# Kernel tuning notes

Measured on AMD Instinct MI355X. Metric: run time of the kernel, lower is better.

The kernel has to match this reference:

```python
import jax, jax.numpy as jnp
import numpy as np

R_RAYS = 65536
S_PER_RAY = 128
N_TOTAL = R_RAYS * S_PER_RAY


def setup_inputs() -> dict:
    key = jax.random.key(0)
    k1, k2, k3, k4 = jax.random.split(key, 4)
    sigmas = jax.random.uniform(k1, (N_TOTAL,), dtype=jnp.float32) * 2.0  # densities >= 0
    rgbs = jax.random.uniform(k2, (N_TOTAL, 3), dtype=jnp.float32)
    deltas = jax.random.uniform(k3, (N_TOTAL,), dtype=jnp.float32) * 0.01 + 1e-3
    ts = jax.random.uniform(k4, (N_TOTAL,), dtype=jnp.float32) * 6.0 + 0.1
    ray_idx = jnp.arange(R_RAYS, dtype=jnp.int32)
    rays_a = jnp.stack([ray_idx, ray_idx * S_PER_RAY,
                        jnp.full((R_RAYS,), S_PER_RAY, dtype=jnp.int32)], axis=1)
    return {"sigmas": sigmas, "rgbs": rgbs, "deltas": deltas, "ts": ts,
            "rays_a": rays_a, "T_threshold": 1e-4}


def reference(sigmas, rgbs, deltas, ts, rays_a, T_threshold):
    R = rays_a.shape[0]
    N = sigmas.shape[0]
    S_max = int(jnp.max(rays_a[:, 2]))  # max samples per ray (concrete)

    offs = jnp.arange(S_max, dtype=rays_a.dtype)
    valid = offs[None, :] < rays_a[:, 2, None]              # [R, S] prefix mask
    idx = jnp.where(valid, rays_a[:, 1, None] + offs[None, :], N - 1)  # [R, S]

    a = 1.0 - jnp.exp(-sigmas[idx] * deltas[idx])           # [R, S] alphas

    # Sequential transmittance recurrence with early-exit (T set to 0 once below threshold)
    def step(T, xs):
        a_s, v_s = xs                                        # [R], [R]
        alive = (T > T_threshold) & v_s
        w = jnp.where(alive, a_s * T, 0.0)
        T = jnp.where(alive, T * (1.0 - a_s), 0.0)
        return T, (w, alive)

    T0 = jnp.ones((R,), sigmas.dtype)
    _, (wT, aliveT) = jax.lax.scan(step, T0, (a.T, valid.T))
    w = wT.T                                                 # [R, S] weights
    alive = aliveT.T

    op_n = jnp.sum(w, axis=1)                                # [R]
    dep_n = jnp.sum(w * ts[idx], axis=1)                     # [R]
    rgb_n = jnp.einsum('rs,rsc->rc', w, rgbs[idx])           # [R, 3]
    cnt_n = jnp.sum(alive, axis=1).astype(jnp.int32)

    ridx = rays_a[:, 0]
    opacity = jnp.zeros((R,), w.dtype).at[ridx].add(op_n)
    depth = jnp.zeros((R,), w.dtype).at[ridx].add(dep_n)
    rgb = jnp.zeros((R, 3), w.dtype).at[ridx].add(rgb_n)
    total_samples = jnp.zeros((R,), jnp.int32).at[ridx].add(cnt_n)
    # invalid slots were mapped to index N-1 with w=0, so .add is safe
    ws = jnp.zeros((N,), w.dtype).at[idx.reshape(-1)].add(w.reshape(-1))

    return total_samples.sum(), opacity, depth, rgb, ws
```

## Files before the change

### kernel.cpp

```cpp
#include <hip/hip_runtime.h>


template<int CTRL, int RM>
__device__ __forceinline__ float dpp_mul1(float v) {
    float t = __int_as_float(__builtin_amdgcn_update_dpp(
        0x3f800000, __float_as_int(v), CTRL, RM, 0xF, false));
    return v * t;
}
template<int CTRL>
__device__ __forceinline__ float dpp_add0(float v) {
    float t = __int_as_float(__builtin_amdgcn_update_dpp(
        0, __float_as_int(v), CTRL, 0xF, 0xF, false));
    return v + t;
}
__device__ __forceinline__ float seg_reduce32(float v) {
    v = dpp_add0<0x101>(v);
    v = dpp_add0<0x102>(v);
    v = dpp_add0<0x104>(v);
    v = dpp_add0<0x108>(v);
    v += __int_as_float(__builtin_amdgcn_ds_swizzle(
            __float_as_int(v), 0x401F));
    return v;
}

typedef float f4a __attribute__((ext_vector_type(4), aligned(4)));

__global__ __launch_bounds__(256) void vr_main(
    const float* __restrict__ sigmas, const float* __restrict__ rgbs,
    const float* __restrict__ deltas, const float* __restrict__ ts,
    const int* __restrict__ rays_a, const float* __restrict__ thr_p,
    float* __restrict__ out, float* __restrict__ cnt_ws,
    int R, int use_ws)
{
    const int wib  = (int)(threadIdx.x >> 6);
    const int wid  = (int)blockIdx.x * 4 + wib;
    const int lane = (int)(threadIdx.x & 63);
    const int half = lane >> 5;
    const int sl   = lane & 31;
    const int ray  = 2 * wid + half;
    const bool inR = ray < R;

    int ridx = 0, start = 0, count = 0;
    if (inR) {
        ridx  = rays_a[3 * ray + 0];
        start = rays_a[3 * ray + 1];
        count = rays_a[3 * ray + 2];
    }
    const float thr = thr_p[0];

    const bool ok = inR && (count == 128) && ((start & 3) == 0);
    const bool fastw = __all(ok);

    float fe[4], tv[4], rr[4], gg[4], bb[4];
    bool  v[4];

    if (fastw) {
        const float4 sg4 = *(const float4*)(sigmas + start + 4 * sl);
        const float4 dt4 = *(const float4*)(deltas + start + 4 * sl);
        const float4 tt4 = *(const float4*)(ts     + start + 4 * sl);
        const float* rg = rgbs + 3 * ((size_t)start + 4 * sl);
        const float4 c0 = *(const float4*)(rg + 0);
        const float4 c1 = *(const float4*)(rg + 4);
        const float4 c2 = *(const float4*)(rg + 8);

        fe[0] = __expf(-sg4.x * dt4.x);
        fe[1] = __expf(-sg4.y * dt4.y);
        fe[2] = __expf(-sg4.z * dt4.z);
        fe[3] = __expf(-sg4.w * dt4.w);
        tv[0] = tt4.x; tv[1] = tt4.y; tv[2] = tt4.z; tv[3] = tt4.w;
        rr[0] = c0.x; gg[0] = c0.y; bb[0] = c0.z;
        rr[1] = c0.w; gg[1] = c1.x; bb[1] = c1.y;
        rr[2] = c1.z; gg[2] = c1.w; bb[2] = c2.x;
        rr[3] = c2.y; gg[3] = c2.z; bb[3] = c2.w;
        v[0] = v[1] = v[2] = v[3] = true;
    } else {
        #pragma unroll
        for (int i = 0; i < 4; ++i) {
            const int s = 4 * sl + i;
            const bool vi = inR && (s < count);
            v[i] = vi;
            float sg = 0.f, dt = 0.f;
            tv[i] = 0.f; rr[i] = 0.f; gg[i] = 0.f; bb[i] = 0.f;
            if (vi) {
                sg = sigmas[start + s];
                dt = deltas[start + s];
                tv[i] = ts[start + s];
                const float* rg = rgbs + 3 * ((size_t)start + s);
                rr[i] = rg[0]; gg[i] = rg[1]; bb[i] = rg[2];
            }
            fe[i] = vi ? __expf(-sg * dt) : 1.f;
        }
    }

    const float fprod = (fe[0] * fe[1]) * (fe[2] * fe[3]);
    float inc = fprod;
    inc = dpp_mul1<0x111, 0xF>(inc);
    inc = dpp_mul1<0x112, 0xF>(inc);
    inc = dpp_mul1<0x114, 0xF>(inc);
    inc = dpp_mul1<0x118, 0xF>(inc);
    inc = dpp_mul1<0x142, 0xA>(inc);

    float T = inc / fprod;

    float w[4];
    float cnt = 0.f;
    #pragma unroll
    for (int i = 0; i < 4; ++i) {
        const bool alive = v[i] && (T > thr);
        const float Tn = T * fe[i];
        w[i] = alive ? (T - Tn) : 0.f;
        cnt += alive ? 1.f : 0.f;
        T = Tn;
    }

    float* wsp = out + 1 + 5 * (size_t)R + (size_t)start + 4 * sl;
    if (fastw) {
        f4a wv; wv.x = w[0]; wv.y = w[1]; wv.z = w[2]; wv.w = w[3];
        *(f4a*)wsp = wv;
    } else {
        #pragma unroll
        for (int i = 0; i < 4; ++i) if (v[i]) wsp[i] = w[i];
    }

    float op  = (w[0] + w[1]) + (w[2] + w[3]);
    float dep = fmaf(w[0], tv[0], fmaf(w[1], tv[1], fmaf(w[2], tv[2], w[3] * tv[3])));
    float cr  = fmaf(w[0], rr[0], fmaf(w[1], rr[1], fmaf(w[2], rr[2], w[3] * rr[3])));
    float cg  = fmaf(w[0], gg[0], fmaf(w[1], gg[1], fmaf(w[2], gg[2], w[3] * gg[3])));
    float cb  = fmaf(w[0], bb[0], fmaf(w[1], bb[1], fmaf(w[2], bb[2], w[3] * bb[3])));

    op  = seg_reduce32(op);
    dep = seg_reduce32(dep);
    cr  = seg_reduce32(cr);
    cg  = seg_reduce32(cg);
    cb  = seg_reduce32(cb);
    cnt = seg_reduce32(cnt);

    if (sl == 0 && inR) {
        out[1 + ridx]             = op;
        out[1 + R + ridx]         = dep;
        out[1 + 2*R + 3*ridx + 0] = cr;
        out[1 + 2*R + 3*ridx + 1] = cg;
        out[1 + 2*R + 3*ridx + 2] = cb;
        if (use_ws) cnt_ws[ray] = cnt;
        else        atomicAdd(&out[0], cnt);
    }
}

__global__ __launch_bounds__(1024) void vr_total(
    const float* __restrict__ cnt_ws, float* __restrict__ out, int R)
{
    __shared__ float sm[16];
    float s = 0.f;
    const int R4 = R & ~3;
    for (int i = (int)threadIdx.x * 4; i < R4; i += 4096) {
        const float4 c = *(const float4*)(cnt_ws + i);
        s += (c.x + c.y) + (c.z + c.w);
    }
    if (threadIdx.x == 0)
        for (int i = R4; i < R; ++i) s += cnt_ws[i];
    #pragma unroll
    for (int d = 32; d; d >>= 1) s += __shfl_xor(s, d, 64);
    if ((threadIdx.x & 63) == 0) sm[threadIdx.x >> 6] = s;
    __syncthreads();
    if (threadIdx.x == 0) {
        float t = 0.f;
        #pragma unroll
        for (int k = 0; k < 16; ++k) t += sm[k];
        out[0] = t;
    }
}

extern "C" void kernel_launch(void* const* d_in, const int* in_sizes, int n_in,
                              void* d_out, int out_size, void* d_ws, size_t ws_size,
                              hipStream_t stream) {
    const float* sigmas = (const float*)d_in[0];
    const float* rgbs   = (const float*)d_in[1];
    const float* deltas = (const float*)d_in[2];
    const float* ts     = (const float*)d_in[3];
    const int*   rays_a = (const int*)d_in[4];
    const float* thr    = (const float*)d_in[5];
    int R = in_sizes[4] / 3;
    float* out = (float*)d_out;
    float* cnt_ws = (float*)d_ws;

    int use_ws = (ws_size >= (size_t)R * sizeof(float)) ? 1 : 0;

    if (!use_ws)
        hipMemsetAsync(d_out, 0, 4, stream);

    int grid = (R + 7) / 8;
    vr_main<<<grid, 256, 0, stream>>>(sigmas, rgbs, deltas, ts, rays_a, thr,
                                      out, cnt_ws, R, use_ws);
    if (use_ws)
        vr_total<<<1, 1024, 0, stream>>>(cnt_ws, out, R);
}
```

Before: 46.31 us.

## Process four rays per wave with software-pipelined loads and inclusive-scan shift

Each wave now handles NIT=4 ray pairs strided across the grid, prefetching the next ray's data while computing the current one, and the grid is shrunk accordingly. The exclusive transmittance prefix is obtained with a DPP row shift of the inclusive product instead of dividing by the lane's own product. Segment reductions switch to an inclusive-scan pattern with results read from lane 31. The aim is to hide memory latency and drop a division, at the cost of higher register pressure and fewer blocks for a bandwidth-bound kernel.

```diff
diff --git a/kernel.cpp b/kernel.cpp
--- a/kernel.cpp
+++ b/kernel.cpp
@@ -1,106 +1,87 @@
 #include <hip/hip_runtime.h>
 
 
-template<int CTRL, int RM>
-__device__ __forceinline__ float dpp_mul1(float v) {
-    float t = __int_as_float(__builtin_amdgcn_update_dpp(
-        0x3f800000, __float_as_int(v), CTRL, RM, 0xF, false));
-    return v * t;
-}
-template<int CTRL>
-__device__ __forceinline__ float dpp_add0(float v) {
-    float t = __int_as_float(__builtin_amdgcn_update_dpp(
-        0, __float_as_int(v), CTRL, 0xF, 0xF, false));
-    return v + t;
-}
-__device__ __forceinline__ float seg_reduce32(float v) {
-    v = dpp_add0<0x101>(v);
-    v = dpp_add0<0x102>(v);
-    v = dpp_add0<0x104>(v);
-    v = dpp_add0<0x108>(v);
-    v += __int_as_float(__builtin_amdgcn_ds_swizzle(
-            __float_as_int(v), 0x401F));
+#define NIT 4
+
+typedef float f4a __attribute__((ext_vector_type(4), aligned(4)));
+
+template<int CTRL, int RM, unsigned OLD>
+__device__ __forceinline__ float dpp_f(float v) {
+    return __int_as_float(__builtin_amdgcn_update_dpp(
+        (int)OLD, __float_as_int(v), CTRL, RM, 0xF, false));
+}
+
+__device__ __forceinline__ float seg_sum32_hi(float v) {
+    v += dpp_f<0x111, 0xF, 0u>(v);
+    v += dpp_f<0x112, 0xF, 0u>(v);
+    v += dpp_f<0x114, 0xF, 0u>(v);
+    v += dpp_f<0x118, 0xF, 0u>(v);
+    v += dpp_f<0x142, 0xA, 0u>(v);
     return v;
 }
 
-typedef float f4a __attribute__((ext_vector_type(4), aligned(4)));
-
-__global__ __launch_bounds__(256) void vr_main(
-    const float* __restrict__ sigmas, const float* __restrict__ rgbs,
-    const float* __restrict__ deltas, const float* __restrict__ ts,
-    const int* __restrict__ rays_a, const float* __restrict__ thr_p,
-    float* __restrict__ out, float* __restrict__ cnt_ws,
-    int R, int use_ws)
-{
-    const int wib  = (int)(threadIdx.x >> 6);
-    const int wid  = (int)blockIdx.x * 4 + wib;
-    const int lane = (int)(threadIdx.x & 63);
-    const int half = lane >> 5;
-    const int sl   = lane & 31;
-    const int ray  = 2 * wid + half;
-    const bool inR = ray < R;
-
-    int ridx = 0, start = 0, count = 0;
-    if (inR) {
-        ridx  = rays_a[3 * ray + 0];
-        start = rays_a[3 * ray + 1];
-        count = rays_a[3 * ray + 2];
-    }
-    const float thr = thr_p[0];
-
-    const bool ok = inR && (count == 128) && ((start & 3) == 0);
-    const bool fastw = __all(ok);
-
-    float fe[4], tv[4], rr[4], gg[4], bb[4];
-    bool  v[4];
-
+struct Ld { float4 sg, dt, tt, c0, c1, c2; };
+
+__device__ __forceinline__ Ld load_ray(
+    const float* __restrict__ sigmas, const float* __restrict__ deltas,
+    const float* __restrict__ ts, const float* __restrict__ rgbs,
+    int start, int count, bool inR, int sl, bool fastw)
+{
+    Ld d;
     if (fastw) {
-        const float4 sg4 = *(const float4*)(sigmas + start + 4 * sl);
-        const float4 dt4 = *(const float4*)(deltas + start + 4 * sl);
-        const float4 tt4 = *(const float4*)(ts     + start + 4 * sl);
+        d.sg = *(const float4*)(sigmas + start + 4 * sl);
+        d.dt = *(const float4*)(deltas + start + 4 * sl);
+        d.tt = *(const float4*)(ts     + start + 4 * sl);
         const float* rg = rgbs + 3 * ((size_t)start + 4 * sl);
-        const float4 c0 = *(const float4*)(rg + 0);
-        const float4 c1 = *(const float4*)(rg + 4);
-        const float4 c2 = *(const float4*)(rg + 8);
-
-        fe[0] = __expf(-sg4.x * dt4.x);
-        fe[1] = __expf(-sg4.y * dt4.y);
-        fe[2] = __expf(-sg4.z * dt4.z);
-        fe[3] = __expf(-sg4.w * dt4.w);
-        tv[0] = tt4.x; tv[1] = tt4.y; tv[2] = tt4.z; tv[3] = tt4.w;
-        rr[0] = c0.x; gg[0] = c0.y; bb[0] = c0.z;
-        rr[1] = c0.w; gg[1] = c1.x; bb[1] = c1.y;
-        rr[2] = c1.z; gg[2] = c1.w; bb[2] = c2.x;
-        rr[3] = c2.y; gg[3] = c2.z; bb[3] = c2.w;
-        v[0] = v[1] = v[2] = v[3] = true;
+        d.c0 = *(const float4*)(rg + 0);
+        d.c1 = *(const float4*)(rg + 4);
+        d.c2 = *(const float4*)(rg + 8);
     } else {
+        float sg[4], dt[4], tt[4], rr[4], gg[4], bb[4];
         #pragma unroll
         for (int i = 0; i < 4; ++i) {
             const int s = 4 * sl + i;
             const bool vi = inR && (s < count);
-            v[i] = vi;
-            float sg = 0.f, dt = 0.f;
-            tv[i] = 0.f; rr[i] = 0.f; gg[i] = 0.f; bb[i] = 0.f;
+            sg[i] = dt[i] = tt[i] = rr[i] = gg[i] = bb[i] = 0.f;
             if (vi) {
-                sg = sigmas[start + s];
-                dt = deltas[start + s];
-                tv[i] = ts[start + s];
+                sg[i] = sigmas[start + s];
+                dt[i] = deltas[start + s];
+                tt[i] = ts[start + s];
                 const float* rg = rgbs + 3 * ((size_t)start + s);
                 rr[i] = rg[0]; gg[i] = rg[1]; bb[i] = rg[2];
             }
-            fe[i] = vi ? __expf(-sg * dt) : 1.f;
         }
-    }
+        d.sg = make_float4(sg[0], sg[1], sg[2], sg[3]);
+        d.dt = make_float4(dt[0], dt[1], dt[2], dt[3]);
+        d.tt = make_float4(tt[0], tt[1], tt[2], tt[3]);
+        d.c0 = make_float4(rr[0], gg[0], bb[0], rr[1]);
+        d.c1 = make_float4(gg[1], bb[1], rr[2], gg[2]);
+        d.c2 = make_float4(bb[2], rr[3], gg[3], bb[3]);
+    }
+    return d;
+}
+
+__device__ __forceinline__ void compute_ray(
+    const Ld& d, int ridx, int start, int count, int ray, bool inR, bool fastw,
+    int sl, float thr, float* __restrict__ out, float* __restrict__ cnt_ws,
+    int R, int use_ws)
+{
+    float fe[4] = { __expf(-d.sg.x * d.dt.x), __expf(-d.sg.y * d.dt.y),
+                    __expf(-d.sg.z * d.dt.z), __expf(-d.sg.w * d.dt.w) };
+    bool v[4];
+    #pragma unroll
+    for (int i = 0; i < 4; ++i) v[i] = inR && (4 * sl + i) < count;
 
     const float fprod = (fe[0] * fe[1]) * (fe[2] * fe[3]);
     float inc = fprod;
-    inc = dpp_mul1<0x111, 0xF>(inc);
-    inc = dpp_mul1<0x112, 0xF>(inc);
-    inc = dpp_mul1<0x114, 0xF>(inc);
-    inc = dpp_mul1<0x118, 0xF>(inc);
-    inc = dpp_mul1<0x142, 0xA>(inc);
-
-    float T = inc / fprod;
+    inc *= dpp_f<0x111, 0xF, 0x3f800000u>(inc);
+    inc *= dpp_f<0x112, 0xF, 0x3f800000u>(inc);
+    inc *= dpp_f<0x114, 0xF, 0x3f800000u>(inc);
+    inc *= dpp_f<0x118, 0xF, 0x3f800000u>(inc);
+    inc *= dpp_f<0x142, 0xA, 0x3f800000u>(inc);
+
+    float ex = dpp_f<0x138, 0xF, 0x3f800000u>(inc);
+    float T = (sl == 0) ? 1.f : ex;
 
     float w[4];
     float cnt = 0.f;
@@ -123,26 +104,75 @@
     }
 
     float op  = (w[0] + w[1]) + (w[2] + w[3]);
-    float dep = fmaf(w[0], tv[0], fmaf(w[1], tv[1], fmaf(w[2], tv[2], w[3] * tv[3])));
-    float cr  = fmaf(w[0], rr[0], fmaf(w[1], rr[1], fmaf(w[2], rr[2], w[3] * rr[3])));
-    float cg  = fmaf(w[0], gg[0], fmaf(w[1], gg[1], fmaf(w[2], gg[2], w[3] * gg[3])));
-    float cb  = fmaf(w[0], bb[0], fmaf(w[1], bb[1], fmaf(w[2], bb[2], w[3] * bb[3])));
-
-    op  = seg_reduce32(op);
-    dep = seg_reduce32(dep);
-    cr  = seg_reduce32(cr);
-    cg  = seg_reduce32(cg);
-    cb  = seg_reduce32(cb);
-    cnt = seg_reduce32(cnt);
-
-    if (sl == 0 && inR) {
-        out[1 + ridx]             = op;
-        out[1 + R + ridx]         = dep;
-        out[1 + 2*R + 3*ridx + 0] = cr;
-        out[1 + 2*R + 3*ridx + 1] = cg;
-        out[1 + 2*R + 3*ridx + 2] = cb;
+    float dep = fmaf(w[0], d.tt.x, fmaf(w[1], d.tt.y, fmaf(w[2], d.tt.z, w[3] * d.tt.w)));
+    float cr  = fmaf(w[0], d.c0.x, fmaf(w[1], d.c0.w, fmaf(w[2], d.c1.z, w[3] * d.c2.y)));
+    float cg  = fmaf(w[0], d.c0.y, fmaf(w[1], d.c1.x, fmaf(w[2], d.c1.w, w[3] * d.c2.z)));
+    float cb  = fmaf(w[0], d.c0.z, fmaf(w[1], d.c1.y, fmaf(w[2], d.c2.x, w[3] * d.c2.w)));
+
+    op  = seg_sum32_hi(op);
+    dep = seg_sum32_hi(dep);
+    cr  = seg_sum32_hi(cr);
+    cg  = seg_sum32_hi(cg);
+    cb  = seg_sum32_hi(cb);
+    cnt = seg_sum32_hi(cnt);
+
+    if (sl == 31 && inR) {
+        out[1 + ridx]                 = op;
+        out[1 + R + ridx]             = dep;
+        out[1 + 2 * R + 3 * ridx + 0] = cr;
+        out[1 + 2 * R + 3 * ridx + 1] = cg;
+        out[1 + 2 * R + 3 * ridx + 2] = cb;
         if (use_ws) cnt_ws[ray] = cnt;
         else        atomicAdd(&out[0], cnt);
+    }
+}
+
+__global__ __launch_bounds__(256) void vr_main(
+    const float* __restrict__ sigmas, const float* __restrict__ rgbs,
+    const float* __restrict__ deltas, const float* __restrict__ ts,
+    const int* __restrict__ rays_a, const float* __restrict__ thr_p,
+    float* __restrict__ out, float* __restrict__ cnt_ws,
+    int R, int use_ws)
+{
+    const int wib  = (int)(threadIdx.x >> 6);
+    const int lane = (int)(threadIdx.x & 63);
+    const int half = lane >> 5;
+    const int sl   = lane & 31;
+    const int wid  = (int)blockIdx.x * 4 + wib;
+    const int wpg  = (int)gridDim.x * 4;
+    const float thr = thr_p[0];
+
+    int ridx[NIT], start[NIT], count[NIT], rayk[NIT];
+    bool inR[NIT], fw[NIT];
+    #pragma unroll
+    for (int k = 0; k < NIT; ++k) {
+        const int ray = 2 * (wid + k * wpg) + half;
+        rayk[k] = ray;
+        inR[k] = ray < R;
+        ridx[k] = start[k] = count[k] = 0;
+        if (inR[k]) {
+            ridx[k]  = rays_a[3 * ray + 0];
+            start[k] = rays_a[3 * ray + 1];
+            count[k] = rays_a[3 * ray + 2];
+        }
+    }
+    #pragma unroll
+    for (int k = 0; k < NIT; ++k)
+        fw[k] = __all(inR[k] && (count[k] == 128) && ((start[k] & 3) == 0));
+
+    Ld A = load_ray(sigmas, deltas, ts, rgbs, start[0], count[0], inR[0], sl, fw[0]);
+    #pragma unroll
+    for (int k = 0; k < NIT; ++k) {
+        if (k + 1 < NIT) {
+            Ld B = load_ray(sigmas, deltas, ts, rgbs,
+                            start[k + 1], count[k + 1], inR[k + 1], sl, fw[k + 1]);
+            compute_ray(A, ridx[k], start[k], count[k], rayk[k], inR[k], fw[k],
+                        sl, thr, out, cnt_ws, R, use_ws);
+            A = B;
+        } else {
+            compute_ray(A, ridx[k], start[k], count[k], rayk[k], inR[k], fw[k],
+                        sl, thr, out, cnt_ws, R, use_ws);
+        }
     }
 }
 
@@ -188,7 +218,8 @@
     if (!use_ws)
         hipMemsetAsync(d_out, 0, 4, stream);
 
-    int grid = (R + 7) / 8;
+    const int raysPerBlock = 8 * NIT;
+    int grid = (R + raysPerBlock - 1) / raysPerBlock;
     vr_main<<<grid, 256, 0, stream>>>(sigmas, rgbs, deltas, ts, rays_a, thr,
                                       out, cnt_ws, R, use_ws);
     if (use_ws)
```

New measurement: 47.73 us. +3.1%, slower.
